# Performance work log

Hardware: AMD Instinct MI355X
Metric: run time of the kernel (lower is better)

Reference implementation:

```python
import jax, jax.numpy as jnp
import numpy as np

B, N, DIN, H, DOUT = 32, 1024, 256, 256, 256
NEG = 9000000000000000.0  # -9e15 masking trick from the original code


def setup_inputs() -> dict:
    key = jax.random.key(0)
    ks = jax.random.split(key, 10)
    x = jax.random.normal(ks[0], (B, N, DIN), dtype=jnp.float32)
    # binary float mask (1 = edge present)
    mask = jax.random.randint(ks[1], (B, N, N), 0, 2).astype(jnp.float32)
    s = 0.02
    Wv = jax.random.normal(ks[2], (DIN, H), dtype=jnp.float32) * s
    bv = jnp.zeros((H,), jnp.float32)
    Wk = jax.random.normal(ks[3], (DIN, H), dtype=jnp.float32) * s
    bk = jnp.zeros((H,), jnp.float32)
    Wq = jax.random.normal(ks[4], (DIN, H), dtype=jnp.float32) * s
    bq = jnp.zeros((H,), jnp.float32)
    Wo = jax.random.normal(ks[5], (H, DOUT), dtype=jnp.float32) * s
    bo = jnp.zeros((DOUT,), jnp.float32)
    return {"x": x, "mask": mask, "Wv": Wv, "bv": bv, "Wk": Wk, "bk": bk,
            "Wq": Wq, "bq": bq, "Wo": Wo, "bo": bo}


def reference(x, mask, Wv, bv, Wk, bk, Wq, bq, Wo, bo):
    # x: [B,N,din], mask: [B,N,N]
    v = jax.nn.relu(x @ Wv + bv)              # [B,N,H]
    q = jax.nn.relu(x @ Wq + bq)              # [B,N,H]
    k = jax.nn.relu(x @ Wk + bk)              # [B,N,H]
    scores = jnp.einsum('bnh,bmh->bnm', q, k)  # QK^T, [B,N,N]
    att = jax.nn.softmax(scores * mask - NEG * (1.0 - mask), axis=-1)
    out = jnp.einsum('bnm,bmh->bnh', att, v)   # AV
    return jax.nn.relu(out @ Wo + bo)          # [B,N,d_out]
```

## Files before the change

kernel.cpp:

```cpp
#include <hip/hip_runtime.h>


typedef __attribute__((ext_vector_type(4))) float    f32x4;
typedef __attribute__((ext_vector_type(8))) short    s16x8;
typedef __attribute__((ext_vector_type(4))) short    s16x4;

__device__ __forceinline__ short f2b(float f) {
    union { float f; unsigned u; } v; v.f = f;
    unsigned r = v.u + 0x7FFFu + ((v.u >> 16) & 1u);
    return (short)(r >> 16);
}

__device__ __forceinline__ void gl_lds16(const short* g, short* l) {
    __builtin_amdgcn_global_load_lds(
        (const __attribute__((address_space(1))) unsigned int*)g,
        (__attribute__((address_space(3))) unsigned int*)l, 16, 0, 0);
}

__global__ void prep_w(const float* __restrict__ Wq, const float* __restrict__ Wk,
                       const float* __restrict__ Wv, const float* __restrict__ Wo,
                       short* __restrict__ Wt) {
    int idx = blockIdx.x * 256 + threadIdx.x;
    int w = idx >> 16, rem = idx & 65535;
    int n = rem >> 8, kk = rem & 255;
    const float* W = (w == 0) ? Wq : (w == 1) ? Wk : (w == 2) ? Wv : Wo;
    Wt[idx] = f2b(W[kk * 256 + n]);
}

__global__ __launch_bounds__(256) void qkv_gemm(
        const float* __restrict__ x, const short* __restrict__ Wt,
        const float* __restrict__ bq, const float* __restrict__ bk, const float* __restrict__ bv,
        short* __restrict__ qO, short* __restrict__ kO, short* __restrict__ vtO) {
    __shared__ short a_lds[128][72];
    __shared__ short b_lds[3][64][72];
    const int tid = threadIdx.x;
    const int bm = blockIdx.x >> 2, bn = blockIdx.x & 3;
    const int s0 = bm * 128, n0 = bn * 64;
    const int wid = tid >> 6, l = tid & 63, lo4 = l & 15, hi4 = l >> 4;
    const int wm = wid >> 1, wn = wid & 1;

    f32x4 acc[3][4][2];
    #pragma unroll
    for (int w = 0; w < 3; ++w)
        #pragma unroll
        for (int mi = 0; mi < 4; ++mi)
            #pragma unroll
            for (int ni = 0; ni < 2; ++ni)
                acc[w][mi][ni] = (f32x4){0.f, 0.f, 0.f, 0.f};

    for (int kt = 0; kt < 4; ++kt) {
        const int k0 = kt * 64;
        #pragma unroll
        for (int i = 0; i < 8; ++i) {
            int ch = i * 256 + tid;
            int row = ch >> 4, c4 = (ch & 15) * 4;
            f32x4 xv = *(const f32x4*)(x + (size_t)(s0 + row) * 256 + k0 + c4);
            s16x4 pk = { f2b(xv.x), f2b(xv.y), f2b(xv.z), f2b(xv.w) };
            *(s16x4*)&a_lds[row][c4] = pk;
        }
        #pragma unroll
        for (int w = 0; w < 3; ++w) {
            #pragma unroll
            for (int i = 0; i < 2; ++i) {
                int ch = i * 256 + tid;
                int n = ch >> 3, c8 = (ch & 7) * 8;
                *(s16x8*)&b_lds[w][n][c8] =
                    *(const s16x8*)(Wt + (size_t)w * 65536 + (size_t)(n0 + n) * 256 + k0 + c8);
            }
        }
        __syncthreads();
        s16x8 af[4][2];
        #pragma unroll
        for (int mi = 0; mi < 4; ++mi)
            #pragma unroll
            for (int kk = 0; kk < 2; ++kk)
                af[mi][kk] = *(s16x8*)&a_lds[wm * 64 + mi * 16 + lo4][kk * 32 + hi4 * 8];
        #pragma unroll
        for (int w = 0; w < 3; ++w)
            #pragma unroll
            for (int ni = 0; ni < 2; ++ni)
                #pragma unroll
                for (int kk = 0; kk < 2; ++kk) {
                    s16x8 bfr = *(s16x8*)&b_lds[w][wn * 32 + ni * 16 + lo4][kk * 32 + hi4 * 8];
                    #pragma unroll
                    for (int mi = 0; mi < 4; ++mi)
                        acc[w][mi][ni] = __builtin_amdgcn_mfma_f32_16x16x32_bf16(
                            af[mi][kk], bfr, acc[w][mi][ni], 0, 0, 0);
                }
        __syncthreads();
    }

    const float* bias[3] = { bq, bk, bv };
    for (int w = 0; w < 3; ++w) {
        #pragma unroll
        for (int mi = 0; mi < 4; ++mi)
            #pragma unroll
            for (int ni = 0; ni < 2; ++ni)
                #pragma unroll
                for (int j = 0; j < 4; ++j) {
                    int r = wm * 64 + mi * 16 + hi4 * 4 + j;
                    int c = wn * 32 + ni * 16 + lo4;
                    float v = acc[w][mi][ni][j] + bias[w][n0 + c];
                    a_lds[r][c] = f2b(fmaxf(v, 0.f));
                }
        __syncthreads();
        if (w == 0) {
            #pragma unroll
            for (int i = 0; i < 4; ++i) {
                int ch = i * 256 + tid;
                int row = ch >> 3, c8 = (ch & 7) * 8;
                *(s16x8*)(qO + (size_t)(s0 + row) * 256 + n0 + c8) = *(s16x8*)&a_lds[row][c8];
            }
        } else if (w == 1) {
            #pragma unroll
            for (int i = 0; i < 4; ++i) {
                int ch = i * 256 + tid;
                int row = ch >> 3, c8 = (ch & 7) * 8;
                int swz = ((c8 >> 3) ^ (row & 7)) * 8;
                *(s16x8*)(kO + (size_t)(s0 + row) * 256 + n0 + swz) = *(s16x8*)&a_lds[row][c8];
            }
        } else {
            int bb = s0 >> 10, nn = s0 & 1023;
            #pragma unroll
            for (int i = 0; i < 4; ++i) {
                int ch = i * 256 + tid;
                int h = ch >> 4, sc = (ch & 15) * 8;
                s16x8 t;
                #pragma unroll
                for (int e = 0; e < 8; ++e) t[e] = a_lds[sc + e][h];
                int cil = sc >> 3;
                int swz = (cil & 8) | ((cil & 7) ^ ((n0 + h) & 7));
                *(s16x8*)(vtO + ((size_t)bb * 256 + n0 + h) * 1024 + nn + swz * 8) = t;
            }
        }
        __syncthreads();
    }
}

__global__ __launch_bounds__(512) void attn(
        const short* __restrict__ q, const short* __restrict__ k,
        const short* __restrict__ vt, const float* __restrict__ mask,
        short* __restrict__ attv) {
    __shared__ short kbuf[2][16384];
    __shared__ short vbuf[2][16384];
    __shared__ short p_lds[8][16][72];
    const int tid = threadIdx.x, wid = tid >> 6, l = tid & 63;
    const int lo4 = l & 15, hi4 = l >> 4;
    const int bid = blockIdx.x;
    const int swz = (bid & 7) * 32 + (bid >> 3);
    const int b = swz >> 3, qb = swz & 7;
    const int q0 = qb * 128 + wid * 16;
    const size_t bq_row = (size_t)b * 1024 + q0;

    const short* kb  = k  + (size_t)b * 1024 * 256;
    const short* vtg = vt + (size_t)b * 256 * 1024;
    const float* mb  = mask + ((size_t)b * 1024 + q0 + hi4 * 4) * 1024 + lo4;

#define STAGE_K(bufi, c0_) do { const short* sg_ = kb + (size_t)(c0_) * 256;          \
    _Pragma("unroll") for (int i_ = 0; i_ < 4; ++i_) { int cb_ = i_ * 512 + wid * 64; \
        gl_lds16(sg_ + (size_t)(cb_ + l) * 8, &kbuf[bufi][cb_ * 8]); } } while (0)
#define STAGE_V(bufi, c0_) do {                                                       \
    _Pragma("unroll") for (int i_ = 0; i_ < 4; ++i_) { int cb_ = i_ * 512 + wid * 64; \
        int ch_ = cb_ + l; int h_ = ch_ >> 3, cc_ = ch_ & 7;                          \
        gl_lds16(vtg + (size_t)h_ * 1024 + (c0_) + cc_ * 8, &vbuf[bufi][cb_ * 8]); } } while (0)
#define LOAD_MASK(dst, c0_) do {                                                      \
    _Pragma("unroll") for (int j_ = 0; j_ < 4; ++j_) {                                \
        const float* mr_ = mb + (size_t)j_ * 1024 + (c0_);                            \
        dst[j_] = (f32x4){ mr_[0], mr_[16], mr_[32], mr_[48] }; } } while (0)

    s16x8 qf[8];
    {
        const short* qp = q + (bq_row + lo4) * 256 + hi4 * 8;
        #pragma unroll
        for (int t = 0; t < 8; ++t) qf[t] = *(const s16x8*)(qp + t * 32);
    }
    f32x4 oacc[16];
    #pragma unroll
    for (int t = 0; t < 16; ++t) oacc[t] = (f32x4){0.f, 0.f, 0.f, 0.f};
    float m_run[4] = { -1e30f, -1e30f, -1e30f, -1e30f };
    float l_run[4] = { 0.f, 0.f, 0.f, 0.f };
    f32x4 mkc[4], mkn[4];

    STAGE_K(0, 0);
    LOAD_MASK(mkc, 0);
    STAGE_V(0, 0);

    for (int t = 0; t < 16; ++t) {
        const int cur = t & 1;
        const int c0 = t * 64;
        if (t < 15) {
            STAGE_K(cur ^ 1, c0 + 64);
            LOAD_MASK(mkn, c0 + 64);
            asm volatile("s_waitcnt vmcnt(40)" ::: "memory");
        } else {
            asm volatile("s_waitcnt vmcnt(20)" ::: "memory");
        }
        __builtin_amdgcn_s_barrier();
        f32x4 s[4];
        #pragma unroll
        for (int ct = 0; ct < 4; ++ct) s[ct] = (f32x4){0.f, 0.f, 0.f, 0.f};
        __builtin_amdgcn_s_setprio(1);
        #pragma unroll
        for (int ct = 0; ct < 4; ++ct) {
            int row = ct * 16 + lo4, rx = row & 7;
            #pragma unroll
            for (int tt = 0; tt < 8; ++tt) {
                int ch = tt * 4 + hi4;
                int sc = (ch & 24) | ((ch & 7) ^ rx);
                s16x8 kf = *(s16x8*)&kbuf[cur][row * 256 + sc * 8];
                s[ct] = __builtin_amdgcn_mfma_f32_16x16x32_bf16(qf[tt], kf, s[ct], 0, 0, 0);
            }
        }
        __builtin_amdgcn_s_setprio(0);
        float sm[4][4];
        #pragma unroll
        for (int j = 0; j < 4; ++j) {
            sm[0][j] = (mkc[j].x != 0.f) ? s[0][j] : -1e30f;
            sm[1][j] = (mkc[j].y != 0.f) ? s[1][j] : -1e30f;
            sm[2][j] = (mkc[j].z != 0.f) ? s[2][j] : -1e30f;
            sm[3][j] = (mkc[j].w != 0.f) ? s[3][j] : -1e30f;
        }
        float scale[4], p[4][4];
        #pragma unroll
        for (int j = 0; j < 4; ++j) {
            float tmx = fmaxf(fmaxf(sm[0][j], sm[1][j]), fmaxf(sm[2][j], sm[3][j]));
            tmx = fmaxf(tmx, __shfl_xor(tmx, 1));
            tmx = fmaxf(tmx, __shfl_xor(tmx, 2));
            tmx = fmaxf(tmx, __shfl_xor(tmx, 4));
            tmx = fmaxf(tmx, __shfl_xor(tmx, 8));
            float mnew = fmaxf(m_run[j], tmx);
            scale[j] = __expf(m_run[j] - mnew);
            m_run[j] = mnew;
            float su = 0.f;
            #pragma unroll
            for (int ct = 0; ct < 4; ++ct) { p[ct][j] = __expf(sm[ct][j] - mnew); su += p[ct][j]; }
            su += __shfl_xor(su, 1);
            su += __shfl_xor(su, 2);
            su += __shfl_xor(su, 4);
            su += __shfl_xor(su, 8);
            l_run[j] = l_run[j] * scale[j] + su;
        }
        #pragma unroll
        for (int tt = 0; tt < 16; ++tt)
            #pragma unroll
            for (int j = 0; j < 4; ++j) oacc[tt][j] *= scale[j];
        #pragma unroll
        for (int ct = 0; ct < 4; ++ct)
            #pragma unroll
            for (int j = 0; j < 4; ++j)
                p_lds[wid][hi4 * 4 + j][ct * 16 + lo4] = f2b(p[ct][j]);
        asm volatile("s_waitcnt lgkmcnt(0)" ::: "memory");
        __builtin_amdgcn_sched_barrier(0);
        s16x8 pa0 = *(s16x8*)&p_lds[wid][lo4][hi4 * 8];
        s16x8 pa1 = *(s16x8*)&p_lds[wid][lo4][32 + hi4 * 8];
        if (t < 15) {
            STAGE_V(cur ^ 1, c0 + 64);
            asm volatile("s_waitcnt vmcnt(24)" ::: "memory");
        } else {
            asm volatile("s_waitcnt vmcnt(0)" ::: "memory");
        }
        __builtin_amdgcn_s_barrier();
        __builtin_amdgcn_s_setprio(1);
        #pragma unroll
        for (int nt = 0; nt < 16; ++nt) {
            int h = nt * 16 + lo4, hx = h & 7;
            s16x8 vf0 = *(s16x8*)&vbuf[cur][h * 64 + (hi4 ^ hx) * 8];
            s16x8 vf1 = *(s16x8*)&vbuf[cur][h * 64 + ((hi4 + 4) ^ hx) * 8];
            oacc[nt] = __builtin_amdgcn_mfma_f32_16x16x32_bf16(pa0, vf0, oacc[nt], 0, 0, 0);
            oacc[nt] = __builtin_amdgcn_mfma_f32_16x16x32_bf16(pa1, vf1, oacc[nt], 0, 0, 0);
        }
        __builtin_amdgcn_s_setprio(0);
        if (t < 15) {
            #pragma unroll
            for (int i = 0; i < 4; ++i) mkc[i] = mkn[i];
        }
    }
    float inv[4];
    #pragma unroll
    for (int j = 0; j < 4; ++j) inv[j] = 1.f / l_run[j];
    #pragma unroll
    for (int g = 0; g < 4; ++g) {
        asm volatile("s_waitcnt lgkmcnt(0)" ::: "memory");
        #pragma unroll
        for (int ntl = 0; ntl < 4; ++ntl)
            #pragma unroll
            for (int j = 0; j < 4; ++j)
                p_lds[wid][hi4 * 4 + j][ntl * 16 + lo4] = f2b(oacc[g * 4 + ntl][j] * inv[j]);
        asm volatile("s_waitcnt lgkmcnt(0)" ::: "memory");
        __builtin_amdgcn_sched_barrier(0);
        s16x8 r0 = *(s16x8*)&p_lds[wid][lo4][hi4 * 16];
        s16x8 r1 = *(s16x8*)&p_lds[wid][lo4][hi4 * 16 + 8];
        short* op = attv + (bq_row + lo4) * 256 + g * 64 + hi4 * 16;
        *(s16x8*)op = r0;
        *(s16x8*)(op + 8) = r1;
    }
#undef STAGE_K
#undef STAGE_V
#undef LOAD_MASK
}

__global__ __launch_bounds__(256) void out_gemm(
        const short* __restrict__ a, const short* __restrict__ Wto,
        const float* __restrict__ bo, float* __restrict__ out) {
    __shared__ short a_lds[128][72];
    __shared__ short b_lds[64][72];
    __shared__ float bounce[128][68];
    const int tid = threadIdx.x;
    const int bm = blockIdx.x >> 2, bn = blockIdx.x & 3;
    const int s0 = bm * 128, n0 = bn * 64;
    const int wid = tid >> 6, l = tid & 63, lo4 = l & 15, hi4 = l >> 4;
    const int wm = wid >> 1, wn = wid & 1;
    f32x4 acc[4][2];
    #pragma unroll
    for (int mi = 0; mi < 4; ++mi)
        #pragma unroll
        for (int ni = 0; ni < 2; ++ni) acc[mi][ni] = (f32x4){0.f, 0.f, 0.f, 0.f};

    for (int kt = 0; kt < 4; ++kt) {
        const int k0 = kt * 64;
        #pragma unroll
        for (int i = 0; i < 4; ++i) {
            int ch = i * 256 + tid;
            int row = ch >> 3, c8 = (ch & 7) * 8;
            *(s16x8*)&a_lds[row][c8] = *(const s16x8*)(a + (size_t)(s0 + row) * 256 + k0 + c8);
        }
        #pragma unroll
        for (int i = 0; i < 2; ++i) {
            int ch = i * 256 + tid;
            int n = ch >> 3, c8 = (ch & 7) * 8;
            *(s16x8*)&b_lds[n][c8] = *(const s16x8*)(Wto + (size_t)(n0 + n) * 256 + k0 + c8);
        }
        __syncthreads();
        s16x8 af[4][2];
        #pragma unroll
        for (int mi = 0; mi < 4; ++mi)
            #pragma unroll
            for (int kk = 0; kk < 2; ++kk)
                af[mi][kk] = *(s16x8*)&a_lds[wm * 64 + mi * 16 + lo4][kk * 32 + hi4 * 8];
        #pragma unroll
        for (int ni = 0; ni < 2; ++ni)
            #pragma unroll
            for (int kk = 0; kk < 2; ++kk) {
                s16x8 bfr = *(s16x8*)&b_lds[wn * 32 + ni * 16 + lo4][kk * 32 + hi4 * 8];
                #pragma unroll
                for (int mi = 0; mi < 4; ++mi)
                    acc[mi][ni] = __builtin_amdgcn_mfma_f32_16x16x32_bf16(
                        af[mi][kk], bfr, acc[mi][ni], 0, 0, 0);
            }
        __syncthreads();
    }
    #pragma unroll
    for (int mi = 0; mi < 4; ++mi)
        #pragma unroll
        for (int ni = 0; ni < 2; ++ni)
            #pragma unroll
            for (int j = 0; j < 4; ++j) {
                int r = wm * 64 + mi * 16 + hi4 * 4 + j;
                int c = wn * 32 + ni * 16 + lo4;
                bounce[r][c] = fmaxf(acc[mi][ni][j] + bo[n0 + c], 0.f);
            }
    __syncthreads();
    #pragma unroll
    for (int i = 0; i < 8; ++i) {
        int ch = i * 256 + tid;
        int row = ch >> 4, c4 = (ch & 15) * 4;
        *(f32x4*)(out + (size_t)(s0 + row) * 256 + n0 + c4) = *(f32x4*)&bounce[row][c4];
    }
}

extern "C" void kernel_launch(void* const* d_in, const int* in_sizes, int n_in,
                              void* d_out, int out_size, void* d_ws, size_t ws_size,
                              hipStream_t stream) {
    const float* x    = (const float*)d_in[0];
    const float* mask = (const float*)d_in[1];
    const float* Wv   = (const float*)d_in[2];
    const float* bv   = (const float*)d_in[3];
    const float* Wk   = (const float*)d_in[4];
    const float* bk   = (const float*)d_in[5];
    const float* Wq   = (const float*)d_in[6];
    const float* bq   = (const float*)d_in[7];
    const float* Wo   = (const float*)d_in[8];
    const float* bo   = (const float*)d_in[9];
    float* out = (float*)d_out;

    char* ws = (char*)d_ws;
    short*    Wt  = (short*)ws;
    short*    qB  = (short*)(ws + (1 << 20));
    short*    kB  = qB  + (size_t)32768 * 256;
    short*    vtB = kB  + (size_t)32768 * 256;
    short*    avB = vtB + (size_t)32768 * 256;
    (void)in_sizes; (void)n_in; (void)out_size; (void)ws_size;

    prep_w<<<1024, 256, 0, stream>>>(Wq, Wk, Wv, Wo, Wt);
    qkv_gemm<<<1024, 256, 0, stream>>>(x, Wt, bq, bk, bv, qB, kB, vtB);
    attn<<<256, 512, 0, stream>>>(qB, kB, vtB, mask, avB);
    out_gemm<<<1024, 256, 0, stream>>>(avB, Wt + 3 * 65536, bo, out);
}
```

Before: 138.5 us.

## Pack float mask into bitmask inside QKV GEMM launch for attention

Odd blocks of the QKV GEMM launch now read the float mask and pack it into 64-bit ballot bitmasks in workspace. The attention kernel then loads one u64 per row group instead of scattered strided floats, with the vmcnt waits retuned to the smaller load count. This reduces the mask traffic and load instructions in the attention inner loop. The cost is one full streaming pass over the 128MB float mask in the fused GEMM launch, plus a 4MB bitmask buffer, so total mask reads stay roughly the same but move to coalesced loads off the attention critical path.

```diff
diff --git a/kernel.cpp b/kernel.cpp
--- a/kernel.cpp
+++ b/kernel.cpp
@@ -4,6 +4,7 @@
 typedef __attribute__((ext_vector_type(4))) float    f32x4;
 typedef __attribute__((ext_vector_type(8))) short    s16x8;
 typedef __attribute__((ext_vector_type(4))) short    s16x4;
+typedef unsigned long long u64;
 
 __device__ __forceinline__ short f2b(float f) {
     union { float f; unsigned u; } v; v.f = f;
@@ -30,13 +31,44 @@
 __global__ __launch_bounds__(256) void qkv_gemm(
         const float* __restrict__ x, const short* __restrict__ Wt,
         const float* __restrict__ bq, const float* __restrict__ bk, const float* __restrict__ bv,
+        const float* __restrict__ mask, u64* __restrict__ mp64,
         short* __restrict__ qO, short* __restrict__ kO, short* __restrict__ vtO) {
     __shared__ short a_lds[128][72];
     __shared__ short b_lds[3][64][72];
     const int tid = threadIdx.x;
-    const int bm = blockIdx.x >> 2, bn = blockIdx.x & 3;
+    const int wid = tid >> 6, l = tid & 63, lo4 = l & 15, hi4 = l >> 4;
+
+    if (blockIdx.x & 1) {
+        const int r0 = (blockIdx.x >> 1) * 32;
+        #pragma unroll
+        for (int o = 0; o < 4; ++o) {
+            f32x4 v[8];
+            #pragma unroll
+            for (int i = 0; i < 8; ++i) {
+                int u = o * 32 + wid * 8 + i;
+                int r = r0 + (u >> 2), ch = u & 3;
+                v[i] = *(const f32x4*)(mask + (size_t)r * 1024 + ch * 256 + l * 4);
+            }
+            #pragma unroll
+            for (int i = 0; i < 8; ++i) {
+                int u = o * 32 + wid * 8 + i;
+                int r = r0 + (u >> 2), ch = u & 3;
+                u64 b0 = __ballot(v[i].x != 0.f);
+                u64 b1 = __ballot(v[i].y != 0.f);
+                u64 b2 = __ballot(v[i].z != 0.f);
+                u64 b3 = __ballot(v[i].w != 0.f);
+                if (l < 4) {
+                    u64 bb = (l == 0) ? b0 : (l == 1) ? b1 : (l == 2) ? b2 : b3;
+                    mp64[(size_t)r * 16 + ch * 4 + l] = bb;
+                }
+            }
+        }
+        return;
+    }
+
+    const int bidx = blockIdx.x >> 1;
+    const int bm = bidx >> 2, bn = bidx & 3;
     const int s0 = bm * 128, n0 = bn * 64;
-    const int wid = tid >> 6, l = tid & 63, lo4 = l & 15, hi4 = l >> 4;
     const int wm = wid >> 1, wn = wid & 1;
 
     f32x4 acc[3][4][2];
@@ -139,7 +171,7 @@
 
 __global__ __launch_bounds__(512) void attn(
         const short* __restrict__ q, const short* __restrict__ k,
-        const short* __restrict__ vt, const float* __restrict__ mask,
+        const short* __restrict__ vt, const u64* __restrict__ mp64,
         short* __restrict__ attv) {
     __shared__ short kbuf[2][16384];
     __shared__ short vbuf[2][16384];
@@ -154,7 +186,7 @@
 
     const short* kb  = k  + (size_t)b * 1024 * 256;
     const short* vtg = vt + (size_t)b * 256 * 1024;
-    const float* mb  = mask + ((size_t)b * 1024 + q0 + hi4 * 4) * 1024 + lo4;
+    const u64* mwb = mp64 + ((size_t)b * 1024 + q0 + hi4 * 4) * 16 + (lo4 & 3);
 
 #define STAGE_K(bufi, c0_) do { const short* sg_ = kb + (size_t)(c0_) * 256;          \
     _Pragma("unroll") for (int i_ = 0; i_ < 4; ++i_) { int cb_ = i_ * 512 + wid * 64; \
@@ -163,10 +195,9 @@
     _Pragma("unroll") for (int i_ = 0; i_ < 4; ++i_) { int cb_ = i_ * 512 + wid * 64; \
         int ch_ = cb_ + l; int h_ = ch_ >> 3, cc_ = ch_ & 7;                          \
         gl_lds16(vtg + (size_t)h_ * 1024 + (c0_) + cc_ * 8, &vbuf[bufi][cb_ * 8]); } } while (0)
-#define LOAD_MASK(dst, c0_) do {                                                      \
-    _Pragma("unroll") for (int j_ = 0; j_ < 4; ++j_) {                                \
-        const float* mr_ = mb + (size_t)j_ * 1024 + (c0_);                            \
-        dst[j_] = (f32x4){ mr_[0], mr_[16], mr_[32], mr_[48] }; } } while (0)
+#define LOAD_MASK(dst, t_) do {                                                       \
+    _Pragma("unroll") for (int j_ = 0; j_ < 4; ++j_)                                  \
+        dst[j_] = mwb[(size_t)j_ * 16 + ((t_) >> 2) * 4]; } while (0)
 
     s16x8 qf[8];
     {
@@ -179,7 +210,7 @@
     for (int t = 0; t < 16; ++t) oacc[t] = (f32x4){0.f, 0.f, 0.f, 0.f};
     float m_run[4] = { -1e30f, -1e30f, -1e30f, -1e30f };
     float l_run[4] = { 0.f, 0.f, 0.f, 0.f };
-    f32x4 mkc[4], mkn[4];
+    u64 mkc[4], mkn[4];
 
     STAGE_K(0, 0);
     LOAD_MASK(mkc, 0);
@@ -190,10 +221,10 @@
         const int c0 = t * 64;
         if (t < 15) {
             STAGE_K(cur ^ 1, c0 + 64);
-            LOAD_MASK(mkn, c0 + 64);
-            asm volatile("s_waitcnt vmcnt(40)" ::: "memory");
+            LOAD_MASK(mkn, t + 1);
+            asm volatile("s_waitcnt vmcnt(16)" ::: "memory");
         } else {
-            asm volatile("s_waitcnt vmcnt(20)" ::: "memory");
+            asm volatile("s_waitcnt vmcnt(8)" ::: "memory");
         }
         __builtin_amdgcn_s_barrier();
         f32x4 s[4];
@@ -212,13 +243,15 @@
             }
         }
         __builtin_amdgcn_s_setprio(0);
+        const unsigned shx = ((unsigned)(t & 3) << 4) | (unsigned)(lo4 >> 2);
         float sm[4][4];
         #pragma unroll
         for (int j = 0; j < 4; ++j) {
-            sm[0][j] = (mkc[j].x != 0.f) ? s[0][j] : -1e30f;
-            sm[1][j] = (mkc[j].y != 0.f) ? s[1][j] : -1e30f;
-            sm[2][j] = (mkc[j].z != 0.f) ? s[2][j] : -1e30f;
-            sm[3][j] = (mkc[j].w != 0.f) ? s[3][j] : -1e30f;
+            unsigned wsx = (unsigned)(mkc[j] >> shx);
+            sm[0][j] = (wsx & 1u)     ? s[0][j] : -1e30f;
+            sm[1][j] = (wsx & 16u)    ? s[1][j] : -1e30f;
+            sm[2][j] = (wsx & 256u)   ? s[2][j] : -1e30f;
+            sm[3][j] = (wsx & 4096u)  ? s[3][j] : -1e30f;
         }
         float scale[4], p[4][4];
         #pragma unroll
@@ -255,7 +288,7 @@
         s16x8 pa1 = *(s16x8*)&p_lds[wid][lo4][32 + hi4 * 8];
         if (t < 15) {
             STAGE_V(cur ^ 1, c0 + 64);
-            asm volatile("s_waitcnt vmcnt(24)" ::: "memory");
+            asm volatile("s_waitcnt vmcnt(12)" ::: "memory");
         } else {
             asm volatile("s_waitcnt vmcnt(0)" ::: "memory");
         }
@@ -384,15 +417,16 @@
     float* out = (float*)d_out;
 
     char* ws = (char*)d_ws;
-    short*    Wt  = (short*)ws;
-    short*    qB  = (short*)(ws + (1 << 20));
-    short*    kB  = qB  + (size_t)32768 * 256;
-    short*    vtB = kB  + (size_t)32768 * 256;
-    short*    avB = vtB + (size_t)32768 * 256;
+    short* Wt   = (short*)ws;
+    u64*   mpW  = (u64*)(ws + (512 << 10));
+    short* qB   = (short*)(ws + (4608 << 10));
+    short* kB   = qB  + (size_t)32768 * 256;
+    short* vtB  = kB  + (size_t)32768 * 256;
+    short* avB  = vtB + (size_t)32768 * 256;
     (void)in_sizes; (void)n_in; (void)out_size; (void)ws_size;
 
     prep_w<<<1024, 256, 0, stream>>>(Wq, Wk, Wv, Wo, Wt);
-    qkv_gemm<<<1024, 256, 0, stream>>>(x, Wt, bq, bk, bv, qB, kB, vtB);
-    attn<<<256, 512, 0, stream>>>(qB, kB, vtB, mask, avB);
+    qkv_gemm<<<2048, 256, 0, stream>>>(x, Wt, bq, bk, bv, mask, mpW, qB, kB, vtB);
+    attn<<<256, 512, 0, stream>>>(qB, kB, vtB, mpW, avB);
     out_gemm<<<1024, 256, 0, stream>>>(avB, Wt + 3 * 65536, bo, out);
 }
```

Result: slower. 158.2 us (+14.2%).
